# Optimization experiments

Hardware: AMD Instinct MI355X
Metric: run time of the kernel (lower is better)

## Reference

```python
import jax, jax.numpy as jnp
import numpy as np

TOP_K = 2
SCALING = 16.0 / 8.0  # alpha / rank


def setup_inputs() -> dict:
    key = jax.random.key(0)
    ks = jax.random.split(key, 9)
    B, V, D, P = 32, 21, 512, 64
    IN, OUT, E, R, H = D * P, 96, 8, 8, 256
    return {
        "x": jax.random.normal(ks[0], (B, V, D, P), jnp.float32),
        "W_base": jax.random.normal(ks[1], (OUT, IN), jnp.float32) * (IN ** -0.5),
        "b_base": jax.random.normal(ks[2], (OUT,), jnp.float32) * 0.01,
        "W1": jax.random.normal(ks[3], (H, D), jnp.float32) * (D ** -0.5),
        "b1": jax.random.normal(ks[4], (H,), jnp.float32) * 0.01,
        "W2": jax.random.normal(ks[5], (E, H), jnp.float32) * (H ** -0.5),
        "b2": jax.random.normal(ks[6], (E,), jnp.float32) * 0.01,
        "lora_A": jax.random.normal(ks[7], (E, R, IN), jnp.float32) * (IN ** -0.5),
        "lora_B": jax.random.normal(ks[8], (E, OUT, R), jnp.float32) * (R ** -0.5),
    }


def reference(x, W_base, b_base, W1, b1, W2, b2, lora_A, lora_B):
    B, V, D, P = x.shape
    E = lora_A.shape[0]
    # FlattenHead: flatten last two dims, then linear (dropout is identity in eval)
    flat = x.reshape(B, V, D * P)                      # [B, V, IN]
    base_out = flat @ W_base.T + b_base                # [B, V, OUT]
    # Router: pool over n_vars then patch dim -> [B, D]
    pooled = x.mean(axis=1).mean(axis=-1)
    h = jax.nn.relu(pooled @ W1.T + b1)
    logits = h @ W2.T + b2                             # [B, E]
    probs = jax.nn.softmax(logits, axis=-1)
    topw, topi = jax.lax.top_k(probs, TOP_K)           # [B, K]
    topw = topw / jnp.clip(topw.sum(-1, keepdims=True), 1e-6)
    # All LoRA experts (matches original dense compute), then weighted combine
    temp = jnp.einsum("bvi,eri->ebvr", flat, lora_A)   # [E, B, V, R]
    delta = jnp.einsum("ebvr,eor->ebvo", temp, lora_B) * SCALING  # [E, B, V, OUT]
    # Scatter top-k weights into dense [B, E] then combine (top-k sparse combine)
    w_full = jnp.zeros((B, E), x.dtype).at[jnp.arange(B)[:, None], topi].add(topw)
    moe_delta = jnp.einsum("be,ebvo->bvo", w_full, delta)
    return base_out + moe_delta, probs
```

## Files before the change

### kernel.cpp

```cpp
#include <hip/hip_runtime.h>

#define B_DIM 32
#define V_DIM 21
#define D_DIM 512
#define P_DIM 64
#define M_TOTAL 672
#define K_TOTAL 32768
#define OUT_DIM 96
#define E_DIM 8
#define R_DIM 8
#define H_DIM 256
#define N_TOTAL 160
#define SCALING 2.0f
#define POOL_SCALE (1.0f / (V_DIM * (float)P_DIM))

#define BM 64
#define BK 32
#define KSPLIT 32
#define K_PER_SPLIT (K_TOTAL / KSPLIT)
#define CHUNKS (K_PER_SPLIT / BK)
#define SMN (M_TOTAL * N_TOTAL)
#define NMB 11
#define RC_ROWS 4

typedef __attribute__((ext_vector_type(4))) float floatx4;
typedef __attribute__((ext_vector_type(8))) short short8;

__device__ __forceinline__ unsigned short f2bf(float f) {
  union { float f; unsigned int u; } v; v.f = f;
  unsigned int u = v.u + (0x7FFFu + ((v.u >> 16) & 1u));
  return (unsigned short)(u >> 16);
}

__device__ __forceinline__ unsigned int cvt_pk_bf16(float lo, float hi) {
  unsigned int r;
  asm("v_cvt_pk_bf16_f32 %0, %1, %2" : "=v"(r) : "v"(lo), "v"(hi));
  return r;
}

__device__ __forceinline__ void gl_lds16(const void* g, void* l) {
  __builtin_amdgcn_global_load_lds(
      (const __attribute__((address_space(1))) void*)g,
      (__attribute__((address_space(3))) void*)l, 16, 0, 0);
}

__global__ __launch_bounds__(256)
void convW_kernel(const float* __restrict__ W_base, const float* __restrict__ lora_A,
                  short* __restrict__ Wb) {
  int gid = blockIdx.x * 256 + threadIdx.x;
  size_t base = (size_t)gid * 8;
  int row = (int)(base >> 15);
  int k = (int)(base & 32767);
  const float* src = (row < OUT_DIM) ? (W_base + ((size_t)row << 15) + k)
                                     : (lora_A + ((size_t)(row - OUT_DIM) << 15) + k);
  floatx4 v0 = ((const floatx4*)src)[0];
  floatx4 v1 = ((const floatx4*)src)[1];
  short8 sv;
  sv[0] = (short)f2bf(v0[0]); sv[1] = (short)f2bf(v0[1]);
  sv[2] = (short)f2bf(v0[2]); sv[3] = (short)f2bf(v0[3]);
  sv[4] = (short)f2bf(v1[0]); sv[5] = (short)f2bf(v1[1]);
  sv[6] = (short)f2bf(v1[2]); sv[7] = (short)f2bf(v1[3]);
  *(short8*)(Wb + base) = sv;
}

__global__ __launch_bounds__(256, 2)
void gemm_kernel(const float* __restrict__ x, const short* __restrict__ Wb,
                 float* __restrict__ P, float* __restrict__ pp) {
  __shared__ __attribute__((aligned(16))) float ldsA[4][BM * BK];
  __shared__ __attribute__((aligned(16))) short ldsB[4][N_TOTAL * BK];
  __shared__ float lds_pool[5 * 16];

  const int tid = threadIdx.x;
  const int mb = blockIdx.x;
  const int m0 = mb * BM;
  const int ky = blockIdx.y;
  const int kbase = ky * K_PER_SPLIT;
  const int lane = tid & 63;
  const int wave = tid >> 6;
  const int quad = lane >> 4;
  const int l16 = lane & 15;
  const int b_first = m0 / V_DIM;
  const int d_first = ky * (K_PER_SPLIT / P_DIM);

  if (tid < 80) lds_pool[tid] = 0.0f;

  const float* srcA[2]; int dstA[2];
  #pragma unroll
  for (int it = 0; it < 2; ++it) {
    int idx = it * 256 + tid;
    int row = idx >> 3, j = idx & 7;
    int m = m0 + row; if (m > M_TOTAL - 1) m = M_TOTAL - 1;
    srcA[it] = x + (size_t)m * K_TOTAL + kbase + ((j ^ (row & 7)) << 2);
    dstA[it] = (it * 256 + (tid & 192)) << 2;
  }
  const short* srcB[3]; int dstB[3];
  #pragma unroll
  for (int it = 0; it < 3; ++it) {
    int idx = it * 256 + tid;
    if (idx < 640) {
      int pair = idx >> 3, s8 = idx & 7;
      int c8 = s8 ^ (pair & 7);
      int row = pair * 2 + (c8 >> 2), j = c8 & 3;
      srcB[it] = Wb + (size_t)row * K_TOTAL + kbase + (j << 3);
      dstB[it] = (it * 256 + (tid & 192)) << 3;
    } else {
      srcB[it] = Wb; dstB[it] = 0;
    }
  }

  const int prow = tid >> 2;
  const int part = tid & 3;
  const int ps1 = (prow + part) & 7;
  const int ps2 = (ps1 + 4) & 7;
  const int pm = m0 + prow;
  const int pool_base = (pm < M_TOTAL) ? ((pm / V_DIM) - b_first) * 16 : -1;

#define ISSUE(c, bb)                                                          \
  {                                                                           \
    _Pragma("unroll")                                                         \
    for (int it = 0; it < 2; ++it)                                            \
      gl_lds16(srcA[it] + (c) * BK, &ldsA[bb][dstA[it]]);                     \
    _Pragma("unroll")                                                         \
    for (int it = 0; it < 2; ++it)                                            \
      gl_lds16(srcB[it] + (c) * BK, &ldsB[bb][dstB[it]]);                     \
    if (tid < 128) gl_lds16(srcB[2] + (c) * BK, &ldsB[bb][dstB[2]]);          \
  }

  floatx4 acc[10];
  #pragma unroll
  for (int nt = 0; nt < 10; ++nt) acc[nt] = (floatx4)(0.0f);

  ISSUE(0, 0);
  ISSUE(1, 1);
  asm volatile("s_waitcnt lgkmcnt(0)" ::: "memory");

  #pragma unroll 4
  for (int c = 0; c < CHUNKS; ++c) {
    const int buf = c & 3;
    if (c + 1 < CHUNKS) {
      if (wave < 2) asm volatile("s_waitcnt vmcnt(5)" ::: "memory");
      else          asm volatile("s_waitcnt vmcnt(4)" ::: "memory");
    } else {
      asm volatile("s_waitcnt vmcnt(0)" ::: "memory");
    }
    __builtin_amdgcn_sched_barrier(0);
    __builtin_amdgcn_s_barrier();
    __builtin_amdgcn_sched_barrier(0);
    if (c + 2 < CHUNKS) ISSUE(c + 2, (c + 2) & 3);
    {
      const floatx4* aT = (const floatx4*)ldsA[buf];
      floatx4 u = aT[prow * 8 + ps1];
      floatx4 w = aT[prow * 8 + ps2];
      float s = ((u[0] + u[1]) + (u[2] + u[3])) + ((w[0] + w[1]) + (w[2] + w[3]));
      s += __shfl_down(s, 2, 4);
      s += __shfl_down(s, 1, 4);
      if (part == 0 && pool_base >= 0)
        atomicAdd(&lds_pool[pool_base + (c >> 1)], s);
    }
    {
      const floatx4* aT = (const floatx4*)ldsA[buf];
      const int r = wave * 16 + l16;
      floatx4 f0 = aT[r * 8 + ((2 * quad) ^ (r & 7))];
      floatx4 f1 = aT[r * 8 + ((2 * quad + 1) ^ (r & 7))];
      union { short8 s; unsigned int u[4]; } av;
      av.u[0] = cvt_pk_bf16(f0[0], f0[1]);
      av.u[1] = cvt_pk_bf16(f0[2], f0[3]);
      av.u[2] = cvt_pk_bf16(f1[0], f1[1]);
      av.u[3] = cvt_pk_bf16(f1[2], f1[3]);
      const short8* bT = (const short8*)ldsB[buf];
      #pragma unroll
      for (int nt = 0; nt < 10; ++nt) {
        int r2 = nt * 16 + l16;
        int pr = r2 >> 1;
        short8 b = bT[pr * 8 + ((((r2 & 1) << 2) | quad) ^ (pr & 7))];
        acc[nt] = __builtin_amdgcn_mfma_f32_16x16x32_bf16(av.s, b, acc[nt], 0, 0, 0);
      }
    }
  }

  __syncthreads();

  {
    const int mrow = m0 + wave * 16 + quad * 4;
    float* Pp = P + (size_t)ky * SMN + (size_t)mrow * N_TOTAL + l16;
    #pragma unroll
    for (int r = 0; r < 4; ++r)
      if (mrow + r < M_TOTAL)
        #pragma unroll
        for (int nt = 0; nt < 10; ++nt)
          Pp[(size_t)r * N_TOTAL + nt * 16] = acc[nt][r];
  }

  if (tid < 80) {
    int bl = tid >> 4, dl = tid & 15;
    pp[((size_t)(mb * 5 + bl)) * D_DIM + d_first + dl] = lds_pool[tid];
  }
}

__global__ __launch_bounds__(256)
void router_kernel(const float* __restrict__ pp, const float* __restrict__ W1,
                   const float* __restrict__ b1, const float* __restrict__ W2,
                   const float* __restrict__ b2, float* __restrict__ wfull,
                   float* __restrict__ probs_out) {
  __shared__ float sp[D_DIM];
  __shared__ float sh[H_DIM];
  __shared__ float slog[E_DIM];
  const int b = blockIdx.x;
  const int t = threadIdx.x;
  const int mb1 = (b * V_DIM) / BM;
  const int mb2 = (b * V_DIM + V_DIM - 1) / BM;
  const int bf1 = (mb1 * BM) / V_DIM;
  const int bf2 = (mb2 * BM) / V_DIM;
  const float* p1 = pp + (size_t)(mb1 * 5 + (b - bf1)) * D_DIM;
  const float* p2 = pp + (size_t)(mb2 * 5 + (b - bf2)) * D_DIM;
  for (int d = t; d < D_DIM; d += 256) {
    float v = p1[d];
    if (mb2 != mb1) v += p2[d];
    sp[d] = v * POOL_SCALE;
  }
  __syncthreads();
  float acc = b1[t];
  const float* w1r = W1 + (size_t)t * D_DIM;
  for (int d = 0; d < D_DIM; ++d) acc += sp[d] * w1r[d];
  sh[t] = fmaxf(acc, 0.0f);
  __syncthreads();
  if (t < E_DIM) {
    float a = b2[t];
    const float* w2r = W2 + t * H_DIM;
    for (int j = 0; j < H_DIM; ++j) a += sh[j] * w2r[j];
    slog[t] = a;
  }
  __syncthreads();
  if (t == 0) {
    float p[E_DIM];
    float mx = slog[0];
    for (int e = 1; e < E_DIM; ++e) mx = fmaxf(mx, slog[e]);
    float se = 0.0f;
    for (int e = 0; e < E_DIM; ++e) { p[e] = __expf(slog[e] - mx); se += p[e]; }
    float inv = 1.0f / se;
    for (int e = 0; e < E_DIM; ++e) { p[e] *= inv; probs_out[b * E_DIM + e] = p[e]; }
    int i0 = 0;
    for (int e = 1; e < E_DIM; ++e) if (p[e] > p[i0]) i0 = e;
    int i1 = (i0 == 0) ? 1 : 0;
    for (int e = 0; e < E_DIM; ++e) if (e != i0 && p[e] > p[i1]) i1 = e;
    float s2 = p[i0] + p[i1];
    float invs = 1.0f / fmaxf(s2, 1e-6f);
    for (int e = 0; e < E_DIM; ++e) {
      float w = 0.0f;
      if (e == i0) w += p[i0] * invs;
      if (e == i1) w += p[i1] * invs;
      wfull[b * E_DIM + e] = w;
    }
  }
}

__global__ __launch_bounds__(256)
void reduce_combine_kernel(const float* __restrict__ P, const float* __restrict__ b_base,
                           const float* __restrict__ lora_B, const float* __restrict__ wfull,
                           float* __restrict__ out) {
  __shared__ float sS[RC_ROWS * N_TOTAL];
  const int t = threadIdx.x;
  const int NF4 = RC_ROWS * N_TOTAL / 4;
  if (t < NF4) {
    const floatx4* P4 = (const floatx4*)P;
    size_t base = (size_t)blockIdx.x * NF4 + t;
    floatx4 a = (floatx4)(0.0f);
    #pragma unroll 8
    for (int k = 0; k < KSPLIT; ++k) a += P4[(size_t)k * (SMN / 4) + base];
    *(floatx4*)&sS[t * 4] = a;
  }
  __syncthreads();
  for (int i = t; i < RC_ROWS * OUT_DIM; i += 256) {
    int mr = i / OUT_DIM;
    int o = i - mr * OUT_DIM;
    int mm = blockIdx.x * RC_ROWS + mr;
    int b = mm / V_DIM;
    const float* srow = sS + mr * N_TOTAL;
    float res = srow[o] + b_base[o];
    float moe = 0.0f;
    #pragma unroll
    for (int e = 0; e < E_DIM; ++e) {
      float we = wfull[b * E_DIM + e];
      if (we != 0.0f) {
        const float* lb = lora_B + ((size_t)e * OUT_DIM + o) * R_DIM;
        float dd = 0.0f;
        #pragma unroll
        for (int r = 0; r < R_DIM; ++r) dd += srow[OUT_DIM + e * R_DIM + r] * lb[r];
        moe += we * dd;
      }
    }
    out[(size_t)mm * OUT_DIM + o] = res + SCALING * moe;
  }
}

extern "C" void kernel_launch(void* const* d_in, const int* in_sizes, int n_in,
                              void* d_out, int out_size, void* d_ws, size_t ws_size,
                              hipStream_t stream) {
  const float* x      = (const float*)d_in[0];
  const float* W_base = (const float*)d_in[1];
  const float* b_base = (const float*)d_in[2];
  const float* W1     = (const float*)d_in[3];
  const float* b1     = (const float*)d_in[4];
  const float* W2     = (const float*)d_in[5];
  const float* b2     = (const float*)d_in[6];
  const float* lora_A = (const float*)d_in[7];
  const float* lora_B = (const float*)d_in[8];
  float* out = (float*)d_out;

  float* ws    = (float*)d_ws;
  float* pp    = ws;
  float* wfull = ws + NMB * 5 * D_DIM;
  short* Wb    = (short*)(wfull + 256);
  float* P     = (float*)(Wb + (size_t)N_TOTAL * K_TOTAL);

  convW_kernel<<<(N_TOTAL * K_TOTAL / 8 + 255) / 256, 256, 0, stream>>>(
      W_base, lora_A, Wb);
  gemm_kernel<<<dim3(NMB, KSPLIT), 256, 0, stream>>>(x, Wb, P, pp);
  router_kernel<<<B_DIM, 256, 0, stream>>>(pp, W1, b1, W2, b2, wfull,
                                           out + (size_t)M_TOTAL * OUT_DIM);
  reduce_combine_kernel<<<M_TOTAL / RC_ROWS, 256, 0, stream>>>(
      P, b_base, lora_B, wfull, out);
}
```

Measured before the change: 215.4 us.

## Load x directly into registers, deepen B pipeline, remap blocks across XCDs

The fp32 x tile no longer goes through LDS. Each lane loads its own A fragment straight from global memory into a four-deep register ring, and the router pooling partial sums are built from those same registers. The B (bf16 weight) LDS pipeline grows from two chunks to three in flight, with hand-written ds_read_b128 loads and explicit waitcnts. The grid is flattened and block IDs are remapped so blocks sharing a K-split land on the same XCD, aiming for better L2 reuse of the weight slices. This cuts LDS traffic and bank conflicts for A, but register pressure goes up and the global A loads are less coalesced (16 rows by 32 bytes per lane).

```diff
diff --git a/kernel.cpp b/kernel.cpp
--- a/kernel.cpp
+++ b/kernel.cpp
@@ -42,6 +42,10 @@
   __builtin_amdgcn_global_load_lds(
       (const __attribute__((address_space(1))) void*)g,
       (__attribute__((address_space(3))) void*)l, 16, 0, 0);
+}
+
+__device__ __forceinline__ short8 as_s8(floatx4 v) {
+  union { floatx4 f; short8 s; } u; u.f = v; return u.s;
 }
 
 __global__ __launch_bounds__(256)
@@ -66,116 +70,129 @@
 __global__ __launch_bounds__(256, 2)
 void gemm_kernel(const float* __restrict__ x, const short* __restrict__ Wb,
                  float* __restrict__ P, float* __restrict__ pp) {
-  __shared__ __attribute__((aligned(16))) float ldsA[4][BM * BK];
   __shared__ __attribute__((aligned(16))) short ldsB[4][N_TOTAL * BK];
   __shared__ float lds_pool[5 * 16];
 
   const int tid = threadIdx.x;
-  const int mb = blockIdx.x;
+  const int bid = blockIdx.x;
+  const int xcd = bid & 7;
+  const int grp = bid >> 3;
+  const int ky  = xcd + 8 * (grp / NMB);
+  const int mb  = grp % NMB;
   const int m0 = mb * BM;
-  const int ky = blockIdx.y;
   const int kbase = ky * K_PER_SPLIT;
   const int lane = tid & 63;
   const int wave = tid >> 6;
   const int quad = lane >> 4;
   const int l16 = lane & 15;
   const int b_first = m0 / V_DIM;
-  const int d_first = ky * (K_PER_SPLIT / P_DIM);
 
   if (tid < 80) lds_pool[tid] = 0.0f;
-
-  const float* srcA[2]; int dstA[2];
-  #pragma unroll
-  for (int it = 0; it < 2; ++it) {
-    int idx = it * 256 + tid;
-    int row = idx >> 3, j = idx & 7;
-    int m = m0 + row; if (m > M_TOTAL - 1) m = M_TOTAL - 1;
-    srcA[it] = x + (size_t)m * K_TOTAL + kbase + ((j ^ (row & 7)) << 2);
-    dstA[it] = (it * 256 + (tid & 192)) << 2;
-  }
-  const short* srcB[3]; int dstB[3];
-  #pragma unroll
-  for (int it = 0; it < 3; ++it) {
-    int idx = it * 256 + tid;
-    if (idx < 640) {
-      int pair = idx >> 3, s8 = idx & 7;
-      int c8 = s8 ^ (pair & 7);
-      int row = pair * 2 + (c8 >> 2), j = c8 & 3;
-      srcB[it] = Wb + (size_t)row * K_TOTAL + kbase + (j << 3);
-      dstB[it] = (it * 256 + (tid & 192)) << 3;
-    } else {
-      srcB[it] = Wb; dstB[it] = 0;
-    }
-  }
-
-  const int prow = tid >> 2;
-  const int part = tid & 3;
-  const int ps1 = (prow + part) & 7;
-  const int ps2 = (ps1 + 4) & 7;
-  const int pm = m0 + prow;
-  const int pool_base = (pm < M_TOTAL) ? ((pm / V_DIM) - b_first) * 16 : -1;
-
-#define ISSUE(c, bb)                                                          \
+  asm volatile("s_waitcnt lgkmcnt(0)" ::: "memory");
+
+  const int arow_raw = m0 + wave * 16 + l16;
+  const bool row_ok = (arow_raw < M_TOTAL);
+  const int arow = row_ok ? arow_raw : (M_TOTAL - 1);
+  const floatx4* aptr =
+      (const floatx4*)(x + (size_t)arow * K_TOTAL + kbase + quad * 8);
+
+  const short* srcB0; const short* srcB1; const short* srcB2 = Wb;
+  int dstB0, dstB1, dstB2 = 0;
+  {
+    int idx = tid, pair = idx >> 3, s8 = idx & 7;
+    srcB0 = Wb + (size_t)(2 * pair + (s8 >> 2)) * K_TOTAL + kbase + (s8 & 3) * 8;
+    dstB0 = (tid & 192) << 3;
+    idx = 256 + tid; pair = idx >> 3; s8 = idx & 7;
+    srcB1 = Wb + (size_t)(2 * pair + (s8 >> 2)) * K_TOTAL + kbase + (s8 & 3) * 8;
+    dstB1 = (256 + (tid & 192)) << 3;
+    if (tid < 128) {
+      idx = 512 + tid; pair = idx >> 3; s8 = idx & 7;
+      srcB2 = Wb + (size_t)(2 * pair + (s8 >> 2)) * K_TOTAL + kbase + (s8 & 3) * 8;
+      dstB2 = (512 + (tid & 192)) << 3;
+    }
+  }
+  const unsigned baddr =
+      (unsigned)(size_t)(__attribute__((address_space(3))) short*)&ldsB[0][0] +
+      (unsigned)((l16 >> 1) * 128 + ((((l16 & 1) << 2) | quad) * 16));
+
+#define ISSUE_B(c, bb)                                                        \
   {                                                                           \
-    _Pragma("unroll")                                                         \
-    for (int it = 0; it < 2; ++it)                                            \
-      gl_lds16(srcA[it] + (c) * BK, &ldsA[bb][dstA[it]]);                     \
-    _Pragma("unroll")                                                         \
-    for (int it = 0; it < 2; ++it)                                            \
-      gl_lds16(srcB[it] + (c) * BK, &ldsB[bb][dstB[it]]);                     \
-    if (tid < 128) gl_lds16(srcB[2] + (c) * BK, &ldsB[bb][dstB[2]]);          \
-  }
-
+    gl_lds16(srcB0 + (c) * BK, &ldsB[bb][dstB0]);                             \
+    gl_lds16(srcB1 + (c) * BK, &ldsB[bb][dstB1]);                             \
+    if (tid < 128) gl_lds16(srcB2 + (c) * BK, &ldsB[bb][dstB2]);              \
+  }
+#define WAITV(N) asm volatile("s_waitcnt vmcnt(" #N ")" ::: "memory")
+#define SBAR __builtin_amdgcn_sched_barrier(0)
+
+  floatx4 af[4][2];
   floatx4 acc[10];
   #pragma unroll
   for (int nt = 0; nt < 10; ++nt) acc[nt] = (floatx4)(0.0f);
-
-  ISSUE(0, 0);
-  ISSUE(1, 1);
-  asm volatile("s_waitcnt lgkmcnt(0)" ::: "memory");
-
-  #pragma unroll 4
+  floatx4 paccv = (floatx4)(0.0f);
+
+  ISSUE_B(0, 0); SBAR;
+  af[0][0] = aptr[0];  af[0][1] = aptr[1];  SBAR;
+  ISSUE_B(1, 1); SBAR;
+  af[1][0] = aptr[8];  af[1][1] = aptr[9];  SBAR;
+  ISSUE_B(2, 2); SBAR;
+  af[2][0] = aptr[16]; af[2][1] = aptr[17];
+  af[3][0] = aptr[24]; af[3][1] = aptr[25];
+
+  #pragma unroll
   for (int c = 0; c < CHUNKS; ++c) {
-    const int buf = c & 3;
-    if (c + 1 < CHUNKS) {
-      if (wave < 2) asm volatile("s_waitcnt vmcnt(5)" ::: "memory");
-      else          asm volatile("s_waitcnt vmcnt(4)" ::: "memory");
-    } else {
-      asm volatile("s_waitcnt vmcnt(0)" ::: "memory");
-    }
-    __builtin_amdgcn_sched_barrier(0);
+    const int bb = c & 3;
+    if (c <= CHUNKS - 4)      { if (wave < 2) WAITV(12); else WAITV(10); }
+    else if (c == CHUNKS - 3) { if (wave < 2) WAITV(10); else WAITV(8); }
+    else if (c == CHUNKS - 2) { if (wave < 2) WAITV(5);  else WAITV(4); }
+    else                      { WAITV(0); }
+    SBAR;
     __builtin_amdgcn_s_barrier();
-    __builtin_amdgcn_sched_barrier(0);
-    if (c + 2 < CHUNKS) ISSUE(c + 2, (c + 2) & 3);
-    {
-      const floatx4* aT = (const floatx4*)ldsA[buf];
-      floatx4 u = aT[prow * 8 + ps1];
-      floatx4 w = aT[prow * 8 + ps2];
-      float s = ((u[0] + u[1]) + (u[2] + u[3])) + ((w[0] + w[1]) + (w[2] + w[3]));
-      s += __shfl_down(s, 2, 4);
-      s += __shfl_down(s, 1, 4);
-      if (part == 0 && pool_base >= 0)
-        atomicAdd(&lds_pool[pool_base + (c >> 1)], s);
-    }
-    {
-      const floatx4* aT = (const floatx4*)ldsA[buf];
-      const int r = wave * 16 + l16;
-      floatx4 f0 = aT[r * 8 + ((2 * quad) ^ (r & 7))];
-      floatx4 f1 = aT[r * 8 + ((2 * quad + 1) ^ (r & 7))];
-      union { short8 s; unsigned int u[4]; } av;
-      av.u[0] = cvt_pk_bf16(f0[0], f0[1]);
-      av.u[1] = cvt_pk_bf16(f0[2], f0[3]);
-      av.u[2] = cvt_pk_bf16(f1[0], f1[1]);
-      av.u[3] = cvt_pk_bf16(f1[2], f1[3]);
-      const short8* bT = (const short8*)ldsB[buf];
-      #pragma unroll
-      for (int nt = 0; nt < 10; ++nt) {
-        int r2 = nt * 16 + l16;
-        int pr = r2 >> 1;
-        short8 b = bT[pr * 8 + ((((r2 & 1) << 2) | quad) ^ (pr & 7))];
-        acc[nt] = __builtin_amdgcn_mfma_f32_16x16x32_bf16(av.s, b, acc[nt], 0, 0, 0);
-      }
-    }
+    SBAR;
+    if (c + 3 < CHUNKS) ISSUE_B(c + 3, (c + 3) & 3);
+    SBAR;
+    floatx4 f0 = af[bb][0], f1 = af[bb][1];
+    union { short8 s; unsigned int u[4]; } av;
+    av.u[0] = cvt_pk_bf16(f0[0], f0[1]);
+    av.u[1] = cvt_pk_bf16(f0[2], f0[3]);
+    av.u[2] = cvt_pk_bf16(f1[0], f1[1]);
+    av.u[3] = cvt_pk_bf16(f1[2], f1[3]);
+    paccv += f0 + f1;
+    if (c & 1) {
+      float h = (paccv[0] + paccv[1]) + (paccv[2] + paccv[3]);
+      h += __shfl_down(h, 32);
+      h += __shfl_down(h, 16);
+      if (lane < 16 && row_ok)
+        atomicAdd(&lds_pool[(arow / V_DIM - b_first) * 16 + (c >> 1)], h);
+      paccv = (floatx4)(0.0f);
+    }
+    if (c + 4 < CHUNKS) {
+      af[bb][0] = aptr[(c + 4) * 8];
+      af[bb][1] = aptr[(c + 4) * 8 + 1];
+    }
+    const unsigned ba = baddr + (unsigned)(bb * (N_TOTAL * BK * 2));
+    floatx4 b0, b1, b2, b3, b4, b5, b6, b7, b8, b9;
+    asm volatile("ds_read_b128 %0, %1 offset:0"    : "=&v"(b0) : "v"(ba));
+    asm volatile("ds_read_b128 %0, %1 offset:1024" : "=&v"(b1) : "v"(ba));
+    asm volatile("ds_read_b128 %0, %1 offset:2048" : "=&v"(b2) : "v"(ba));
+    asm volatile("ds_read_b128 %0, %1 offset:3072" : "=&v"(b3) : "v"(ba));
+    asm volatile("ds_read_b128 %0, %1 offset:4096" : "=&v"(b4) : "v"(ba));
+    asm volatile("ds_read_b128 %0, %1 offset:5120" : "=&v"(b5) : "v"(ba));
+    asm volatile("ds_read_b128 %0, %1 offset:6144" : "=&v"(b6) : "v"(ba));
+    asm volatile("ds_read_b128 %0, %1 offset:7168" : "=&v"(b7) : "v"(ba));
+    asm volatile("ds_read_b128 %0, %1 offset:8192" : "=&v"(b8) : "v"(ba));
+    asm volatile("ds_read_b128 %0, %1 offset:9216" : "=&v"(b9) : "v"(ba));
+    asm volatile("s_waitcnt lgkmcnt(0)" ::: "memory");
+    SBAR;
+    acc[0] = __builtin_amdgcn_mfma_f32_16x16x32_bf16(av.s, as_s8(b0), acc[0], 0, 0, 0);
+    acc[1] = __builtin_amdgcn_mfma_f32_16x16x32_bf16(av.s, as_s8(b1), acc[1], 0, 0, 0);
+    acc[2] = __builtin_amdgcn_mfma_f32_16x16x32_bf16(av.s, as_s8(b2), acc[2], 0, 0, 0);
+    acc[3] = __builtin_amdgcn_mfma_f32_16x16x32_bf16(av.s, as_s8(b3), acc[3], 0, 0, 0);
+    acc[4] = __builtin_amdgcn_mfma_f32_16x16x32_bf16(av.s, as_s8(b4), acc[4], 0, 0, 0);
+    acc[5] = __builtin_amdgcn_mfma_f32_16x16x32_bf16(av.s, as_s8(b5), acc[5], 0, 0, 0);
+    acc[6] = __builtin_amdgcn_mfma_f32_16x16x32_bf16(av.s, as_s8(b6), acc[6], 0, 0, 0);
+    acc[7] = __builtin_amdgcn_mfma_f32_16x16x32_bf16(av.s, as_s8(b7), acc[7], 0, 0, 0);
+    acc[8] = __builtin_amdgcn_mfma_f32_16x16x32_bf16(av.s, as_s8(b8), acc[8], 0, 0, 0);
+    acc[9] = __builtin_amdgcn_mfma_f32_16x16x32_bf16(av.s, as_s8(b9), acc[9], 0, 0, 0);
   }
 
   __syncthreads();
@@ -193,7 +210,7 @@
 
   if (tid < 80) {
     int bl = tid >> 4, dl = tid & 15;
-    pp[((size_t)(mb * 5 + bl)) * D_DIM + d_first + dl] = lds_pool[tid];
+    pp[((size_t)(mb * 5 + bl)) * D_DIM + ky * 16 + dl] = lds_pool[tid];
   }
 }
 
@@ -315,7 +332,7 @@
 
   convW_kernel<<<(N_TOTAL * K_TOTAL / 8 + 255) / 256, 256, 0, stream>>>(
       W_base, lora_A, Wb);
-  gemm_kernel<<<dim3(NMB, KSPLIT), 256, 0, stream>>>(x, Wb, P, pp);
+  gemm_kernel<<<NMB * KSPLIT, 256, 0, stream>>>(x, Wb, P, pp);
   router_kernel<<<B_DIM, 256, 0, stream>>>(pp, W1, b1, W2, b2, wfull,
                                            out + (size_t)M_TOTAL * OUT_DIM);
   reduce_combine_kernel<<<M_TOTAL / RC_ROWS, 256, 0, stream>>>(
```

Result: no change. 214.6 us (-0.4%).
